# Kernel optimization log

Measured on AMD Instinct MI355X. Metric: run time of the kernel, lower is better.

The kernel has to match this reference:

```python
import jax, jax.numpy as jnp
import numpy as np

B, N, E, H = 256, 256, 256, 512


def setup_inputs() -> dict:
    key = jax.random.key(0)
    ks = jax.random.split(key, 8)
    sH = 1.0 / np.sqrt(H)  # torch default init scale for LSTMCell / Linear fan_in
    sE = 1.0 / np.sqrt(E)
    return {
        "encoder_output": jax.random.normal(ks[0], (B, N, E), dtype=jnp.float32),
        "W_ih": jax.random.uniform(ks[1], (4 * H, E), jnp.float32, -sH, sH),
        "W_hh": jax.random.uniform(ks[2], (4 * H, H), jnp.float32, -sH, sH),
        "b_ih": jax.random.uniform(ks[3], (4 * H,), jnp.float32, -sH, sH),
        "b_hh": jax.random.uniform(ks[4], (4 * H,), jnp.float32, -sH, sH),
        "W_q": jax.random.uniform(ks[5], (H, H), jnp.float32, -sH, sH),
        "W_k": jax.random.uniform(ks[6], (H, E), jnp.float32, -sE, sE),
        "v": jax.random.uniform(ks[7], (H,), jnp.float32, -sH, sH),
        "max_steps": 256,
    }


def reference(encoder_output, W_ih, W_hh, b_ih, b_hh, W_q, W_k, v, max_steps):
    b, n, e = encoder_output.shape
    h_dim = W_hh.shape[1]
    # W_k(encoder_output) is loop-invariant -> hoist (same math as original)
    k_enc = jnp.einsum("bne,he->bnh", encoder_output, W_k)  # (B, N, H)
    keys = jax.random.split(jax.random.key(42), max_steps)
    batch_idx = jnp.arange(b)

    def step(carry, key):
        h, c, start, visited_mask = carry
        # torch LSTMCell: gates in i, f, g, o order
        gates = start @ W_ih.T + b_ih + h @ W_hh.T + b_hh  # (B, 4H)
        i, f, g, o = jnp.split(gates, 4, axis=-1)
        c = jax.nn.sigmoid(f) * c + jax.nn.sigmoid(i) * jnp.tanh(g)
        h = jax.nn.sigmoid(o) * jnp.tanh(c)
        q = h @ W_q.T  # (B, H)
        scores = jnp.einsum("bnh,h->bn", jnp.tanh(q[:, None, :] + k_enc), v)
        scores = scores - 1.0e6 * visited_mask
        probs = jax.nn.softmax(scores, axis=-1)
        # multinomial(probs, 1) == categorical over masked scores (logits)
        idx = jax.random.categorical(key, scores)  # (B,) int
        action_prob = jnp.take_along_axis(probs, idx[:, None], axis=1)[:, 0]
        visited_mask = visited_mask.at[batch_idx, idx].set(1.0)
        start = encoder_output[batch_idx, idx]  # (B, E)
        return (h, c, start, visited_mask), (idx, action_prob)

    init = (
        jnp.zeros((b, h_dim), jnp.float32),
        jnp.zeros((b, h_dim), jnp.float32),
        jnp.zeros((b, e), jnp.float32),
        jnp.zeros((b, n), jnp.float32),
    )
    _, (seq, action_probs) = jax.lax.scan(step, init, keys)
    action_sequence = seq.T  # (B, max_steps)
    logp_sum = jnp.sum(action_probs, axis=0)  # (B,) -- sums probs, as original does
    return action_sequence, logp_sum
```

## Files before the change

### kernel.cpp

```cpp
#include <hip/hip_runtime.h>
#include <cstdint>
#include <math.h>

typedef unsigned int u32;

#define BB 256
#define NN 256
#define EE 256
#define HH 512
#define G4 2048
#define KK 768
#define TT 256
#define NBLK 256
#define NTHR 1024

#define ALOADD(p)    __hip_atomic_load((p), __ATOMIC_RELAXED, __HIP_MEMORY_SCOPE_AGENT)
#define ASTORED(p,v) __hip_atomic_store((p), (v), __ATOMIC_RELAXED, __HIP_MEMORY_SCOPE_AGENT)
#define ALOADI(p)    __hip_atomic_load((p), __ATOMIC_RELAXED, __HIP_MEMORY_SCOPE_AGENT)
#define ASTOREI(p,v) __hip_atomic_store((p), (v), __ATOMIC_RELAXED, __HIP_MEMORY_SCOPE_AGENT)

__device__ __forceinline__ u32 rotl(u32 x, int d) { return (x << d) | (x >> (32 - d)); }

__device__ __forceinline__ void tf4(u32& x0, u32& x1, int r0, int r1, int r2, int r3) {
  x0 += x1; x1 = rotl(x1, r0); x1 ^= x0;
  x0 += x1; x1 = rotl(x1, r1); x1 ^= x0;
  x0 += x1; x1 = rotl(x1, r2); x1 ^= x0;
  x0 += x1; x1 = rotl(x1, r3); x1 ^= x0;
}

__device__ __forceinline__ void threefry2x32(u32 k0, u32 k1, u32 x0, u32 x1, u32& o0, u32& o1) {
  u32 k2 = k0 ^ k1 ^ 0x1BD11BDAu;
  x0 += k0; x1 += k1;
  tf4(x0, x1, 13, 15, 26, 6);  x0 += k1; x1 += k2 + 1u;
  tf4(x0, x1, 17, 29, 16, 24); x0 += k2; x1 += k0 + 2u;
  tf4(x0, x1, 13, 15, 26, 6);  x0 += k0; x1 += k1 + 3u;
  tf4(x0, x1, 17, 29, 16, 24); x0 += k1; x1 += k2 + 4u;
  tf4(x0, x1, 13, 15, 26, 6);  x0 += k2; x1 += k0 + 5u;
  o0 = x0; o1 = x1;
}

struct Args {
  const float *enc, *W_ih, *W_hh, *b_ih, *b_hh, *W_q, *W_k, *v;
  float *out;
  float *kT;
  float *Wc;
  float *WqT;
  double *bsum;
  u32 *keys;
  double *h0, *h1;
  double *c;
  double *q;
  int *idx;
  u32 *flags;
};

__device__ __forceinline__ void grid_barrier(u32* cnt, u32* gen) {
  __syncthreads();
  if (threadIdx.x == 0) {
    u32 g = __hip_atomic_load(gen, __ATOMIC_RELAXED, __HIP_MEMORY_SCOPE_AGENT);
    __threadfence();
    if (atomicAdd(cnt, 1u) == NBLK - 1u) {
      __hip_atomic_store(cnt, 0u, __ATOMIC_RELAXED, __HIP_MEMORY_SCOPE_AGENT);
      __threadfence();
      atomicAdd(gen, 1u);
    } else {
      while (__hip_atomic_load(gen, __ATOMIC_RELAXED, __HIP_MEMORY_SCOPE_AGENT) == g) {
        __builtin_amdgcn_s_sleep(2);
      }
    }
    __threadfence();
  }
  __syncthreads();
}

__device__ __forceinline__ void pod_signal(u32* ph, int pod, int me, u32 val) {
  asm volatile("s_waitcnt vmcnt(0)" ::: "memory");
  __syncthreads();
  if (threadIdx.x == 0) ASTOREI(&ph[pod * 32 + me], val);
}
__device__ __forceinline__ void pod_wait(u32* ph, int pod, u32 target) {
  const int t = threadIdx.x;
  if (t < 32) {
    while (ALOADI(&ph[pod * 32 + t]) < target) { __builtin_amdgcn_s_sleep(1); }
  }
  __syncthreads();
}

__global__ __launch_bounds__(NTHR) void mono_kernel(Args a) {
  const int blk = blockIdx.x;
  const int t = threadIdx.x;
  __shared__ alignas(16) unsigned char SMRAW[42368];
  __shared__ int visS[NN];
  __shared__ float vSp[HH];
  __shared__ double logpS;
  const int grp = blk >> 5;
  const int me  = blk & 31;
  const int jb = 4 * (blk & 7) + ((blk >> 3) & 3);
  u32* p1f = a.flags;
  u32* qf  = a.flags + 256;
  u32* p2f = a.flags + 512;

  {
    const int tid = blk * NTHR + t;
    const int tot = NBLK * NTHR;
    if (tid < BB * HH) { a.h0[tid] = 0.0; a.c[tid] = 0.0; }
    if (tid < BB) a.idx[tid] = -1;
    if (tid < 256) {
      u32 o0, o1;
      threefry2x32(0u, 42u, 0u, (u32)tid, o0, o1);
      a.keys[2 * tid] = o0; a.keys[2 * tid + 1] = o1;
    }
    if (tid < G4) a.bsum[tid] = (double)a.b_ih[tid] + (double)a.b_hh[tid];
    for (int i = tid; i < HH * HH; i += tot) {
      int h2 = i >> 9, h = i & 511;
      a.WqT[i] = a.W_q[h * HH + h2];
    }
    for (int i = tid; i < KK * G4; i += tot) {
      int k = i >> 11, col = i & 2047;
      int x16 = col >> 6, g = (col >> 4) & 3, w = col & 15;
      int j = g * HH + x16 * 16 + w;
      a.Wc[i] = (k < EE) ? a.W_ih[j * EE + k] : a.W_hh[j * HH + (k - EE)];
    }
    if (t < NN) visS[t] = 0;
    if (t < HH) vSp[t] = a.v[t];
    if (t == 0) logpS = 0.0;
  }
  {
    float (*encS)[65] = (float(*)[65])SMRAW;
    float (*wkS)[65]  = (float(*)[65])(SMRAW + 64 * 65 * 4);
    const int tn = t & 63, th = t >> 6;
    for (int tile = blk; tile < 8 * 4 * BB; tile += NBLK) {
      const int bx = tile & 7, by = (tile >> 3) & 3, b = tile >> 5;
      const int h0i = bx * 64, n0 = by * 64;
      double acc[4];
#pragma unroll
      for (int i = 0; i < 4; i++) acc[i] = 0.0;
      for (int ec = 0; ec < EE; ec += 64) {
        __syncthreads();
#pragma unroll
        for (int i = 0; i < 4; i++) {
          int idx = i * NTHR + t; int r = idx >> 6, cc = idx & 63;
          encS[r][cc] = a.enc[((size_t)b * NN + n0 + r) * EE + ec + cc];
          wkS[r][cc]  = a.W_k[(size_t)(h0i + r) * EE + ec + cc];
        }
        __syncthreads();
#pragma unroll 8
        for (int e = 0; e < 64; e++) {
          double ev = (double)encS[tn][e];
#pragma unroll
          for (int i = 0; i < 4; i++) acc[i] += (double)wkS[th * 4 + i][e] * ev;
        }
      }
#pragma unroll
      for (int i = 0; i < 4; i++)
        a.kT[((size_t)b * HH + h0i + th * 4 + i) * NN + n0 + tn] = (float)acc[i];
    }
  }
  grid_barrier(a.flags + 768, a.flags + 800);

  for (int step = 0; step < TT; step++) {
    double* hPrev = (step & 1) ? a.h1 : a.h0;
    double* hCur  = (step & 1) ? a.h0 : a.h1;
    const int b0 = grp * 32;

    if (step > 0) pod_wait(p2f, grp, (u32)step);

    {
      double (*aS)[33] = (double(*)[33])SMRAW;
      double (*bS)[66] = (double(*)[66])(SMRAW + 8448);
      int* idxP = (int*)(SMRAW + 25344);
      const int sr = t >> 5, scp = t & 31;
      const int bk = t >> 6, bc = t & 63;
      if (t < 32) idxP[t] = ALOADI(&a.idx[b0 + t]);
      __syncthreads();

      double aR; float bR0, bR1;
      {
        int iv = idxP[sr];
        aR = (iv >= 0) ? (double)a.enc[((size_t)(b0 + sr) * NN + iv) * EE + scp] : 0.0;
        bR0 = a.Wc[(size_t)(bk)      * G4 + jb * 64 + bc];
        bR1 = a.Wc[(size_t)(bk + 16) * G4 + jb * 64 + bc];
      }
      const int jc = t & 63, rg2 = t >> 6;
      double acc0, acc1, acc2, acc3;
      {
        double bv = a.bsum[(jc >> 4) * HH + jb * 16 + (jc & 15)];
        acc0 = bv; acc1 = bv; acc2 = bv; acc3 = bv;
      }
      for (int kc = 0; kc < KK; kc += 32) {
        aS[sr][scp] = aR;
        bS[bk][bc]      = (double)bR0;
        bS[bk + 16][bc] = (double)bR1;
        int kn = kc + 32;
        if (kn < KK) {
          if (kn < EE) {
            int iv = idxP[sr];
            aR = (iv >= 0) ? (double)a.enc[((size_t)(b0 + sr) * NN + iv) * EE + kn + scp] : 0.0;
          } else {
            aR = ALOADD(&hPrev[(size_t)(b0 + sr) * HH + (kn - EE) + scp]);
          }
          bR0 = a.Wc[(size_t)(kn + bk)      * G4 + jb * 64 + bc];
          bR1 = a.Wc[(size_t)(kn + bk + 16) * G4 + jb * 64 + bc];
        }
        __syncthreads();
        if (t < 512) {
#pragma unroll 8
          for (int kk = 0; kk < 32; kk++) {
            double bv = bS[kk][jc];
            acc0 += aS[rg2 * 4][kk]     * bv;
            acc1 += aS[rg2 * 4 + 1][kk] * bv;
            acc2 += aS[rg2 * 4 + 2][kk] * bv;
            acc3 += aS[rg2 * 4 + 3][kk] * bv;
          }
        }
        __syncthreads();
      }
      double (*gS)[66] = (double(*)[66])SMRAW;
      if (t < 512) {
        gS[rg2 * 4][jc]     = acc0;
        gS[rg2 * 4 + 1][jc] = acc1;
        gS[rg2 * 4 + 2][jc] = acc2;
        gS[rg2 * 4 + 3][jc] = acc3;
      }
      __syncthreads();
      if (t < 512) {
        const int b = t >> 4, w = t & 15;
        double ig = gS[b][w], fg = gS[b][16 + w], gv = gS[b][32 + w], og = gS[b][48 + w];
        double si = 1.0 / (1.0 + exp(-ig));
        double sf = 1.0 / (1.0 + exp(-fg));
        double so = 1.0 / (1.0 + exp(-og));
        size_t ci = (size_t)(b0 + b) * HH + jb * 16 + w;
        double cn = sf * a.c[ci] + si * tanh(gv);
        a.c[ci] = cn;
        ASTORED(&hCur[ci], so * tanh(cn));
      }
    }
    pod_signal(p1f, grp, me, (u32)(step + 1));
    pod_wait(p1f, grp, (u32)(step + 1));

    {
      double (*hS)[33] = (double(*)[33])SMRAW;
      float  (*wS)[17] = (float (*)[17])(SMRAW + 8448);
      const int sr = t >> 5, scp = t & 31;
      const int wk = t >> 4, wj = t & 15;
      const int j0 = jb * 16;
      double hR = ALOADD(&hCur[(size_t)(b0 + sr) * HH + scp]);
      float  wR = (t < 512) ? a.WqT[(size_t)wk * HH + j0 + wj] : 0.0f;
      const int bq = t >> 4, j = t & 15;
      double p0 = 0.0, p1 = 0.0, p2 = 0.0, p3 = 0.0;
      for (int kc = 0; kc < HH; kc += 32) {
        hS[sr][scp] = hR;
        if (t < 512) wS[wk][wj] = wR;
        int kn = kc + 32;
        if (kn < HH) {
          hR = ALOADD(&hCur[(size_t)(b0 + sr) * HH + kn + scp]);
          if (t < 512) wR = a.WqT[(size_t)(kn + wk) * HH + j0 + wj];
        }
        __syncthreads();
        if (t < 512) {
#pragma unroll 8
          for (int kk = 0; kk < 32; kk += 4) {
            p0 += hS[bq][kk]     * (double)wS[kk][j];
            p1 += hS[bq][kk + 1] * (double)wS[kk + 1][j];
            p2 += hS[bq][kk + 2] * (double)wS[kk + 2][j];
            p3 += hS[bq][kk + 3] * (double)wS[kk + 3][j];
          }
        }
        __syncthreads();
      }
      if (t < 512)
        ASTORED(&a.q[(size_t)(b0 + bq) * HH + j0 + j], (p0 + p1) + (p2 + p3));
    }
    pod_signal(qf, grp, me, (u32)(step + 1));
    pod_wait(qf, grp, (u32)(step + 1));

    {
      double* qS  = (double*)SMRAW;
      double* pS  = (double*)(SMRAW + 4096);
      double* sS  = (double*)(SMRAW + 37120);
      double* red = (double*)(SMRAW + 39168);
      int*   redi = (int*)(SMRAW + 41216);
      int*   idxS = (int*)(SMRAW + 42240);
      const int b = blk;
      if (t < 512) qS[t] = ALOADD(&a.q[(size_t)b * HH + t]);
      __syncthreads();

      const int col4 = (t & 63) * 4, slice = t >> 6;
      const float* kp = a.kT + ((size_t)b * HH + slice * 32) * NN + col4;
      double c0 = 0.0, c1 = 0.0, c2 = 0.0, c3 = 0.0;
#pragma unroll 4
      for (int h = 0; h < 32; h++) {
        float4 kv = *(const float4*)(kp + (size_t)h * NN);
        int hh = slice * 32 + h;
        double qh = qS[hh];
        double vh = (double)vSp[hh];
        c0 += vh * (double)tanhf((float)(qh + (double)kv.x));
        c1 += vh * (double)tanhf((float)(qh + (double)kv.y));
        c2 += vh * (double)tanhf((float)(qh + (double)kv.z));
        c3 += vh * (double)tanhf((float)(qh + (double)kv.w));
      }
      {
        double* pw = pS + slice * 258 + col4;
        pw[0] = c0; pw[1] = c1; pw[2] = c2; pw[3] = c3;
      }
      __syncthreads();

      if (t < 256) {
        double s = 0.0;
#pragma unroll
        for (int sl = 0; sl < 16; sl++) s += pS[sl * 258 + t];
        if (visS[t]) s -= 1.0e6;
        sS[t] = s;
      }
      __syncthreads();

      if (t < 256) {
        u32 fl = (u32)(b * 256 + t);
        u32 o0, o1;
        threefry2x32(a.keys[2 * step], a.keys[2 * step + 1], 0u, fl, o0, o1);
        u32 bits = o0 ^ o1;
        u32 fb = (bits >> 9) | 0x3F800000u;
        float uf = __uint_as_float(fb) - 1.0f;
        double uu = (uf > 0.0f) ? (double)uf : (double)1.17549435e-38f;
        double gmb = -log(-log(uu));
        red[t] = gmb + sS[t];
        redi[t] = t;
      }
      __syncthreads();
      for (int s2 = 128; s2 > 0; s2 >>= 1) {
        if (t < s2) {
          double v1 = red[t], v2 = red[t + s2];
          int i1 = redi[t], i2 = redi[t + s2];
          if (v2 > v1 || (v2 == v1 && i2 < i1)) { red[t] = v2; redi[t] = i2; }
        }
        __syncthreads();
      }
      if (t == 0) *idxS = redi[0];

      if (t < 256) red[t] = sS[t];
      __syncthreads();
      for (int s2 = 128; s2 > 0; s2 >>= 1) {
        if (t < s2) red[t] = fmax(red[t], red[t + s2]);
        __syncthreads();
      }
      double m = red[0];
      __syncthreads();
      if (t < 256) red[t] = exp(sS[t] - m);
      __syncthreads();
      for (int s2 = 128; s2 > 0; s2 >>= 1) {
        if (t < s2) red[t] += red[t + s2];
        __syncthreads();
      }
      if (t == 0) {
        int bi = *idxS;
        double p = exp(sS[bi] - m) / red[0];
        logpS += p;
        a.out[(size_t)b * TT + step] = (float)bi;
        visS[bi] = 1;
        ASTOREI(&a.idx[b], bi);
      }
    }
    pod_signal(p2f, grp, me, (u32)(step + 1));
  }

  if (t == 0) a.out[BB * TT + blk] = (float)logpS;
}

extern "C" void kernel_launch(void* const* d_in, const int* in_sizes, int n_in,
                              void* d_out, int out_size, void* d_ws, size_t ws_size,
                              hipStream_t stream) {
  char* ws = (char*)d_ws;
  Args a;
  a.enc  = (const float*)d_in[0];
  a.W_ih = (const float*)d_in[1];
  a.W_hh = (const float*)d_in[2];
  a.b_ih = (const float*)d_in[3];
  a.b_hh = (const float*)d_in[4];
  a.W_q  = (const float*)d_in[5];
  a.W_k  = (const float*)d_in[6];
  a.v    = (const float*)d_in[7];
  a.out  = (float*)d_out;

  a.kT    = (float*)(ws + 0);
  a.Wc    = (float*)(ws + 134217728);
  a.WqT   = (float*)(ws + 140509184);
  a.bsum  = (double*)(ws + 141557760);
  a.keys  = (u32*)(ws + 141574144);
  a.h0    = (double*)(ws + 141576192);
  a.h1    = (double*)(ws + 142624768);
  a.c     = (double*)(ws + 143673344);
  a.idx   = (int*)(ws + 144721920);
  a.flags = (u32*)(ws + 144723968);
  a.q     = (double*)(ws + 144728064);

  hipMemsetAsync((void*)a.flags, 0, 4096, stream);

  void* kargs[] = { &a };
  hipLaunchCooperativeKernel(reinterpret_cast<void*>(&mono_kernel),
                             dim3(NBLK), dim3(NTHR), kargs, 0, stream);
}
```

Baseline: 29.10 ms.

## Overlap h-part of gate GEMM with pod wait and signal before softmax

Splits the per-step gate GEMM so the W_hh·h part (which depends on hPrev) runs before waiting on the inter-block pod flag, and only the W_ih·x part that needs the sampled index waits. It also publishes the sampled index and signals the pod right after the argmax, before the max/exp/sum softmax reductions used only for the action probability. Both aim to shorten the cross-block critical path in this persistent grid-synchronised loop. The risk is that hPrev must already be complete without the wait, and the extra __syncthreads add some cost.

```diff
diff --git a/kernel.cpp b/kernel.cpp
--- a/kernel.cpp
+++ b/kernel.cpp
@@ -163,42 +163,62 @@
     double* hCur  = (step & 1) ? a.h0 : a.h1;
     const int b0 = grp * 32;
 
-    if (step > 0) pod_wait(p2f, grp, (u32)step);
-
     {
       double (*aS)[33] = (double(*)[33])SMRAW;
       double (*bS)[66] = (double(*)[66])(SMRAW + 8448);
       int* idxP = (int*)(SMRAW + 25344);
       const int sr = t >> 5, scp = t & 31;
       const int bk = t >> 6, bc = t & 63;
+      const int jc = t & 63, rg2 = t >> 6;
+      double acc0, acc1, acc2, acc3;
+      {
+        double bv = a.bsum[(jc >> 4) * HH + jb * 16 + (jc & 15)];
+        acc0 = bv; acc1 = bv; acc2 = bv; acc3 = bv;
+      }
+      double aR; float bR0, bR1;
+      aR  = ALOADD(&hPrev[(size_t)(b0 + sr) * HH + scp]);
+      bR0 = a.Wc[(size_t)(EE + bk)      * G4 + jb * 64 + bc];
+      bR1 = a.Wc[(size_t)(EE + bk + 16) * G4 + jb * 64 + bc];
+      for (int kc = EE; kc < KK; kc += 32) {
+        aS[sr][scp] = aR;
+        bS[bk][bc]      = (double)bR0;
+        bS[bk + 16][bc] = (double)bR1;
+        int kn = kc + 32;
+        if (kn < KK) {
+          aR  = ALOADD(&hPrev[(size_t)(b0 + sr) * HH + (kn - EE) + scp]);
+          bR0 = a.Wc[(size_t)(kn + bk)      * G4 + jb * 64 + bc];
+          bR1 = a.Wc[(size_t)(kn + bk + 16) * G4 + jb * 64 + bc];
+        }
+        __syncthreads();
+        if (t < 512) {
+#pragma unroll 8
+          for (int kk = 0; kk < 32; kk++) {
+            double bv = bS[kk][jc];
+            acc0 += aS[rg2 * 4][kk]     * bv;
+            acc1 += aS[rg2 * 4 + 1][kk] * bv;
+            acc2 += aS[rg2 * 4 + 2][kk] * bv;
+            acc3 += aS[rg2 * 4 + 3][kk] * bv;
+          }
+        }
+        __syncthreads();
+      }
+      pod_wait(p2f, grp, (u32)step);
       if (t < 32) idxP[t] = ALOADI(&a.idx[b0 + t]);
       __syncthreads();
-
-      double aR; float bR0, bR1;
       {
         int iv = idxP[sr];
         aR = (iv >= 0) ? (double)a.enc[((size_t)(b0 + sr) * NN + iv) * EE + scp] : 0.0;
         bR0 = a.Wc[(size_t)(bk)      * G4 + jb * 64 + bc];
         bR1 = a.Wc[(size_t)(bk + 16) * G4 + jb * 64 + bc];
       }
-      const int jc = t & 63, rg2 = t >> 6;
-      double acc0, acc1, acc2, acc3;
-      {
-        double bv = a.bsum[(jc >> 4) * HH + jb * 16 + (jc & 15)];
-        acc0 = bv; acc1 = bv; acc2 = bv; acc3 = bv;
-      }
-      for (int kc = 0; kc < KK; kc += 32) {
+      for (int kc = 0; kc < EE; kc += 32) {
         aS[sr][scp] = aR;
         bS[bk][bc]      = (double)bR0;
         bS[bk + 16][bc] = (double)bR1;
         int kn = kc + 32;
-        if (kn < KK) {
-          if (kn < EE) {
-            int iv = idxP[sr];
-            aR = (iv >= 0) ? (double)a.enc[((size_t)(b0 + sr) * NN + iv) * EE + kn + scp] : 0.0;
-          } else {
-            aR = ALOADD(&hPrev[(size_t)(b0 + sr) * HH + (kn - EE) + scp]);
-          }
+        if (kn < EE) {
+          int iv = idxP[sr];
+          aR = (iv >= 0) ? (double)a.enc[((size_t)(b0 + sr) * NN + iv) * EE + kn + scp] : 0.0;
           bR0 = a.Wc[(size_t)(kn + bk)      * G4 + jb * 64 + bc];
           bR1 = a.Wc[(size_t)(kn + bk + 16) * G4 + jb * 64 + bc];
         }
@@ -336,6 +356,14 @@
         __syncthreads();
       }
       if (t == 0) *idxS = redi[0];
+      __syncthreads();
+
+      if (t == 0) {
+        int bi = *idxS;
+        visS[bi] = 1;
+        ASTOREI(&a.idx[b], bi);
+      }
+      pod_signal(p2f, grp, me, (u32)(step + 1));
 
       if (t < 256) red[t] = sS[t];
       __syncthreads();
@@ -356,11 +384,9 @@
         double p = exp(sS[bi] - m) / red[0];
         logpS += p;
         a.out[(size_t)b * TT + step] = (float)bi;
-        visS[bi] = 1;
-        ASTOREI(&a.idx[b], bi);
-      }
-    }
-    pod_signal(p2f, grp, me, (u32)(step + 1));
+      }
+      __syncthreads();
+    }
   }
 
   if (t == 0) a.out[BB * TT + blk] = (float)logpS;
```

Result: no change. 29.42 ms (+1.1%).

## Deepen load prefetch and signal sampled index before softmax probability

Applied to the files above, without the earlier changes.

The gate GEMM loop now prefetches two k-chunks ahead using a two-slot register queue instead of one, and the attention score loop preloads eight float4 key rows ahead to hide global memory latency. The per-step pod signal that releases the next LSTM step is moved earlier, right after the sampled index is chosen and published, so the softmax max/sum reductions for the action probability overlap with the next step's wait. This costs more registers per thread and adds an extra block barrier.

```diff
diff --git a/kernel.cpp b/kernel.cpp
--- a/kernel.cpp
+++ b/kernel.cpp
@@ -174,13 +174,20 @@
       if (t < 32) idxP[t] = ALOADI(&a.idx[b0 + t]);
       __syncthreads();
 
-      double aR; float bR0, bR1;
-      {
-        int iv = idxP[sr];
-        aR = (iv >= 0) ? (double)a.enc[((size_t)(b0 + sr) * NN + iv) * EE + scp] : 0.0;
-        bR0 = a.Wc[(size_t)(bk)      * G4 + jb * 64 + bc];
-        bR1 = a.Wc[(size_t)(bk + 16) * G4 + jb * 64 + bc];
-      }
+      double aRq[2]; float bR0q[2], bR1q[2];
+      auto issueA = [&](int kc, int slot) {
+        if (kc < EE) {
+          int iv = idxP[sr];
+          aRq[slot] = (iv >= 0) ? (double)a.enc[((size_t)(b0 + sr) * NN + iv) * EE + kc + scp] : 0.0;
+        } else {
+          aRq[slot] = ALOADD(&hPrev[(size_t)(b0 + sr) * HH + (kc - EE) + scp]);
+        }
+        bR0q[slot] = a.Wc[(size_t)(kc + bk)      * G4 + jb * 64 + bc];
+        bR1q[slot] = a.Wc[(size_t)(kc + bk + 16) * G4 + jb * 64 + bc];
+      };
+      issueA(0, 0);
+      issueA(32, 1);
+
       const int jc = t & 63, rg2 = t >> 6;
       double acc0, acc1, acc2, acc3;
       {
@@ -188,20 +195,11 @@
         acc0 = bv; acc1 = bv; acc2 = bv; acc3 = bv;
       }
       for (int kc = 0; kc < KK; kc += 32) {
-        aS[sr][scp] = aR;
-        bS[bk][bc]      = (double)bR0;
-        bS[bk + 16][bc] = (double)bR1;
-        int kn = kc + 32;
-        if (kn < KK) {
-          if (kn < EE) {
-            int iv = idxP[sr];
-            aR = (iv >= 0) ? (double)a.enc[((size_t)(b0 + sr) * NN + iv) * EE + kn + scp] : 0.0;
-          } else {
-            aR = ALOADD(&hPrev[(size_t)(b0 + sr) * HH + (kn - EE) + scp]);
-          }
-          bR0 = a.Wc[(size_t)(kn + bk)      * G4 + jb * 64 + bc];
-          bR1 = a.Wc[(size_t)(kn + bk + 16) * G4 + jb * 64 + bc];
-        }
+        const int slot = (kc >> 5) & 1;
+        aS[sr][scp] = aRq[slot];
+        bS[bk][bc]      = (double)bR0q[slot];
+        bS[bk + 16][bc] = (double)bR1q[slot];
+        if (kc + 64 < KK) issueA(kc + 64, slot);
         __syncthreads();
         if (t < 512) {
 #pragma unroll 8
@@ -288,16 +286,23 @@
       const int col4 = (t & 63) * 4, slice = t >> 6;
       const float* kp = a.kT + ((size_t)b * HH + slice * 32) * NN + col4;
       double c0 = 0.0, c1 = 0.0, c2 = 0.0, c3 = 0.0;
-#pragma unroll 4
-      for (int h = 0; h < 32; h++) {
-        float4 kv = *(const float4*)(kp + (size_t)h * NN);
-        int hh = slice * 32 + h;
-        double qh = qS[hh];
-        double vh = (double)vSp[hh];
-        c0 += vh * (double)tanhf((float)(qh + (double)kv.x));
-        c1 += vh * (double)tanhf((float)(qh + (double)kv.y));
-        c2 += vh * (double)tanhf((float)(qh + (double)kv.z));
-        c3 += vh * (double)tanhf((float)(qh + (double)kv.w));
+      float4 kv[8];
+#pragma unroll
+      for (int i = 0; i < 8; i++) kv[i] = *(const float4*)(kp + (size_t)i * NN);
+#pragma unroll
+      for (int hb = 0; hb < 32; hb += 8) {
+#pragma unroll
+        for (int i = 0; i < 8; i++) {
+          float4 cur = kv[i];
+          if (hb + 8 < 32) kv[i] = *(const float4*)(kp + (size_t)(hb + 8 + i) * NN);
+          int hh = slice * 32 + hb + i;
+          double qh = qS[hh];
+          double vh = (double)vSp[hh];
+          c0 += vh * (double)tanhf((float)(qh + (double)cur.x));
+          c1 += vh * (double)tanhf((float)(qh + (double)cur.y));
+          c2 += vh * (double)tanhf((float)(qh + (double)cur.z));
+          c3 += vh * (double)tanhf((float)(qh + (double)cur.w));
+        }
       }
       {
         double* pw = pS + slice * 258 + col4;
@@ -336,6 +341,14 @@
         __syncthreads();
       }
       if (t == 0) *idxS = redi[0];
+      __syncthreads();
+
+      if (t == 0) {
+        int bi = *idxS;
+        visS[bi] = 1;
+        ASTOREI(&a.idx[b], bi);
+      }
+      pod_signal(p2f, grp, me, (u32)(step + 1));
 
       if (t < 256) red[t] = sS[t];
       __syncthreads();
@@ -356,11 +369,9 @@
         double p = exp(sS[bi] - m) / red[0];
         logpS += p;
         a.out[(size_t)b * TT + step] = (float)bi;
-        visS[bi] = 1;
-        ASTOREI(&a.idx[b], bi);
-      }
-    }
-    pod_signal(p2f, grp, me, (u32)(step + 1));
+      }
+      __syncthreads();
+    }
   }
 
   if (t == 0) a.out[BB * TT + blk] = (float)logpS;
```

Measured after the change: 88.33 ms. +203.5%, slower.
